# Kernel tuning notes

Measured on AMD Instinct MI355X. Metric: run time of the kernel, lower is better.

Reference implementation:

```python
import jax, jax.numpy as jnp
import numpy as np

V, E, H, L, B, T = 32000, 256, 512, 128, 16, 128


def _gru_scan(x_emb, h0, W_ih, b_ih, W_hh, b_hh):
    # x_emb: [T, B, E] time-major; torch GRU gate order (r, z, n)
    gx = jnp.einsum('tbe,ge->tbg', x_emb, W_ih) + b_ih  # [T, B, 3H]
    def step(h, g):
        gh = h @ W_hh.T + b_hh
        xr, xz, xn = jnp.split(g, 3, axis=-1)
        hr, hz, hn = jnp.split(gh, 3, axis=-1)
        r = jax.nn.sigmoid(xr + hr)
        u = jax.nn.sigmoid(xz + hz)
        n = jnp.tanh(xn + r * hn)
        h_new = (1.0 - u) * n + u * h
        return h_new, h_new
    return jax.lax.scan(step, h0, gx)


def setup_inputs() -> dict:
    key = jax.random.key(0)
    ks = jax.random.split(key, 20)
    s = 0.02
    f = lambda k, shp: jax.random.normal(k, shp, dtype=jnp.float32) * s
    return {
        'x': jax.random.randint(ks[0], (B, T), 0, V),
        'enc_emb': f(ks[1], (V, E)),
        'enc_W_ih': f(ks[2], (3 * H, E)),
        'enc_b_ih': f(ks[3], (3 * H,)),
        'enc_W_hh': f(ks[4], (3 * H, H)),
        'enc_b_hh': f(ks[5], (3 * H,)),
        'fc_enc_W': f(ks[6], (L, H)),
        'fc_enc_b': f(ks[7], (L,)),
        'fc_dec_W': f(ks[8], (H, L)),
        'fc_dec_b': f(ks[9], (H,)),
        'dec_emb': f(ks[10], (V, E)),
        'dec_W_ih': f(ks[11], (3 * H, E)),
        'dec_b_ih': f(ks[12], (3 * H,)),
        'dec_W_hh': f(ks[13], (3 * H, H)),
        'dec_b_hh': f(ks[14], (3 * H,)),
        'dec_fc_W': f(ks[15], (V, H)),
        'dec_fc_b': f(ks[16], (V,)),
    }


def reference(x, enc_emb, enc_W_ih, enc_b_ih, enc_W_hh, enc_b_hh,
              fc_enc_W, fc_enc_b, fc_dec_W, fc_dec_b,
              dec_emb, dec_W_ih, dec_b_ih, dec_W_hh, dec_b_hh,
              dec_fc_W, dec_fc_b):
    Bx, Tx = x.shape
    Hh = enc_W_hh.shape[1]
    # Encoder: GRU over full sequence, take final hidden
    xe = enc_emb[x].transpose(1, 0, 2)                    # [T, B, E]
    h_last, _ = _gru_scan(xe, jnp.zeros((Bx, Hh), xe.dtype),
                          enc_W_ih, enc_b_ih, enc_W_hh, enc_b_hh)
    z = h_last @ fc_enc_W.T + fc_enc_b                    # [B, L]
    hid0 = jnp.tanh(z @ fc_dec_W.T + fc_dec_b)            # [B, H]
    # Decoder with teacher_forcing=1.0: inputs are x[:, 0:T-1]
    de = dec_emb[x[:, :-1]].transpose(1, 0, 2)            # [T-1, B, E]
    _, hs = _gru_scan(de, hid0, dec_W_ih, dec_b_ih, dec_W_hh, dec_b_hh)
    logits = jnp.einsum('tbh,vh->btv', hs, dec_fc_W) + dec_fc_b  # [B, T-1, V]
    Vv = dec_fc_W.shape[0]
    outputs = jnp.zeros((Bx, Tx, Vv), logits.dtype).at[:, 1:].set(logits)
    return outputs, z
```

## Files before the change

kernel.cpp:

```cpp
#include <hip/hip_runtime.h>

#define Vv 32000
#define Ee 256
#define Hh 512
#define Ll 128
#define Bb 16
#define Tt 128
#define G3 1536
#define NSW 256
#define NPAIRB (Bb * Hh)

typedef __attribute__((ext_vector_type(8))) short short8;
typedef __attribute__((ext_vector_type(4))) float f32x4;

__device__ __forceinline__ float sigmoidf_(float x) { return 1.f / (1.f + __expf(-x)); }

__device__ __forceinline__ unsigned short f2bf(float f) {
  unsigned int u = __float_as_uint(f);
  u = (u + 0x7fffu + ((u >> 16) & 1u)) >> 16;
  return (unsigned short)u;
}

__global__ void k_zero_first(float* __restrict__ out) {
  int idx = blockIdx.x * 256 + threadIdx.x;
  if (idx < Bb * Vv) {
    int b = idx / Vv, v = idx % Vv;
    out[(size_t)b * Tt * Vv + v] = 0.f;
  }
}

__global__ void k_cvt_bf16(const float* __restrict__ in, unsigned short* __restrict__ out,
                           int n4) {
  int i = blockIdx.x * 256 + threadIdx.x;
  if (i < n4) {
    float4 v = ((const float4*)in)[i];
    ushort4 o;
    o.x = f2bf(v.x); o.y = f2bf(v.y); o.z = f2bf(v.z); o.w = f2bf(v.w);
    ((ushort4*)out)[i] = o;
  }
}

__global__ void k_transpose(const float* __restrict__ in, float* __restrict__ out,
                            int R, int C) {
  __shared__ float tile[32][33];
  int c = blockIdx.x * 32 + threadIdx.x;
  int r0 = blockIdx.y * 32;
  for (int i = threadIdx.y; i < 32; i += 8)
    tile[i][threadIdx.x] = in[(size_t)(r0 + i) * C + c];
  __syncthreads();
  int r = r0 + threadIdx.x;
  int c0 = blockIdx.x * 32;
  for (int i = threadIdx.y; i < 32; i += 8)
    out[(size_t)(c0 + i) * R + r] = tile[threadIdx.x][i];
}

__device__ __forceinline__ void gx_body(int e, const int* __restrict__ x,
                                        const float* __restrict__ emb,
                                        const float* __restrict__ WihT,
                                        const float* __restrict__ b_ih,
                                        float* __restrict__ gx) {
  __shared__ float A[16][Ee];
  int mt = e / 6, gy = e % 6;
  int g = gy * 256 + threadIdx.x;
  for (int i = 0; i < 16; i++) {
    int tok = x[i * Tt + mt];
    A[i][threadIdx.x] = emb[(size_t)tok * Ee + threadIdx.x];
  }
  __syncthreads();
  float acc[16];
  float bg = b_ih[g];
#pragma unroll
  for (int i = 0; i < 16; i++) acc[i] = bg;
#pragma unroll 4
  for (int ee = 0; ee < Ee; ee++) {
    float w = WihT[(size_t)ee * G3 + g];
#pragma unroll
    for (int i = 0; i < 16; i++) acc[i] = fmaf(A[i][ee], w, acc[i]);
  }
#pragma unroll
  for (int i = 0; i < 16; i++)
    gx[(size_t)(mt * 16 + i) * G3 + g] = acc[i];
}

__global__ void k_gx(const int* __restrict__ x, const float* __restrict__ emb,
                     const float* __restrict__ WihT, const float* __restrict__ b_ih,
                     float* __restrict__ gx) {
  gx_body(blockIdx.x, x, emb, WihT, b_ih, gx);
}

template <bool HSEQ>
__device__ __forceinline__ void scan_body(
    const float* __restrict__ Whh, const float* __restrict__ bhh,
    const float* __restrict__ gx, uint2* __restrict__ pairs,
    unsigned short* __restrict__ hseq, int nsteps) {
  __shared__ float h_lds[Hh];
  const int tid = threadIdx.x;
  const int wg = blockIdx.x;
  const int g = wg >> 4;
  const int wgl = wg & 15;
  const int wave = tid >> 6;
  const int lane = tid & 63;
  const int cl = lane >> 3;
  const int ks = lane & 7;
  const int j = wgl * 32 + wave * 8 + cl;
  const bool gate = (ks == 0);

  float wr[64], wz[64], wn[64];
  {
    const float* R = Whh + (size_t)j * Hh + ks * 4;
    const float* Z = R + (size_t)Hh * Hh;
    const float* N = Z + (size_t)Hh * Hh;
#pragma unroll
    for (int q = 0; q < 16; ++q) {
      float4 a = *(const float4*)(R + q * 32);
      float4 b = *(const float4*)(Z + q * 32);
      float4 c = *(const float4*)(N + q * 32);
      wr[4*q] = a.x; wr[4*q+1] = a.y; wr[4*q+2] = a.z; wr[4*q+3] = a.w;
      wz[4*q] = b.x; wz[4*q+1] = b.y; wz[4*q+2] = b.z; wz[4*q+3] = b.w;
      wn[4*q] = c.x; wn[4*q+1] = c.y; wn[4*q+2] = c.z; wn[4*q+3] = c.w;
    }
  }
  float bhr = 0.f, bhz = 0.f, bhn = 0.f;
  if (gate) { bhr = bhh[j]; bhz = bhh[Hh + j]; bhn = bhh[2 * Hh + j]; }

  float xr = 0.f, xz = 0.f, xn = 0.f;
  if (gate) {
    const float* gp = gx + (size_t)g * G3 + j;
    xr = gp[0]; xz = gp[Hh]; xn = gp[2 * Hh];
  }

  for (int t = 0; t < nsteps; ++t) {
    {
      const uint4* pp =
          (const uint4*)(pairs + (size_t)(t & 1) * NPAIRB + (size_t)g * Hh) + tid;
      const unsigned ep = (unsigned)t;
      uint4 v;
      for (int it = 0; it < 200000; ++it) {
        asm volatile("global_load_dwordx4 %0, %1, off sc1\n\ts_waitcnt vmcnt(0)"
                     : "=v"(v) : "v"(pp) : "memory");
        if (v.y == ep && v.w == ep) break;
      }
      *(float2*)&h_lds[2 * tid] =
          make_float2(__uint_as_float(v.x), __uint_as_float(v.z));
    }
    __syncthreads();

    float aR = 0.f, aZ = 0.f, aN = 0.f;
    {
      const float* hb = h_lds + ks * 4;
#pragma unroll
      for (int q = 0; q < 16; ++q) {
        float4 hv = *(const float4*)(hb + q * 32);
        aR = fmaf(wr[4*q+0], hv.x, aR);
        aR = fmaf(wr[4*q+1], hv.y, aR);
        aR = fmaf(wr[4*q+2], hv.z, aR);
        aR = fmaf(wr[4*q+3], hv.w, aR);
        aZ = fmaf(wz[4*q+0], hv.x, aZ);
        aZ = fmaf(wz[4*q+1], hv.y, aZ);
        aZ = fmaf(wz[4*q+2], hv.z, aZ);
        aZ = fmaf(wz[4*q+3], hv.w, aZ);
        aN = fmaf(wn[4*q+0], hv.x, aN);
        aN = fmaf(wn[4*q+1], hv.y, aN);
        aN = fmaf(wn[4*q+2], hv.z, aN);
        aN = fmaf(wn[4*q+3], hv.w, aN);
      }
    }
    aR += __shfl_xor(aR, 1, 64); aR += __shfl_xor(aR, 2, 64); aR += __shfl_xor(aR, 4, 64);
    aZ += __shfl_xor(aZ, 1, 64); aZ += __shfl_xor(aZ, 2, 64); aZ += __shfl_xor(aZ, 4, 64);
    aN += __shfl_xor(aN, 1, 64); aN += __shfl_xor(aN, 2, 64); aN += __shfl_xor(aN, 4, 64);

    if (gate) {
      float r = sigmoidf_(xr + aR + bhr);
      float u = sigmoidf_(xz + aZ + bhz);
      float n = tanhf(xn + r * (aN + bhn));
      float hold = h_lds[j];
      float hnew = (1.f - u) * n + u * hold;
      uint2 pv = make_uint2(__float_as_uint(hnew), (unsigned)(t + 1));
      uint2* dst = pairs + (size_t)((t + 1) & 1) * NPAIRB + (size_t)g * Hh + j;
      asm volatile("global_store_dwordx2 %0, %1, off sc1" : : "v"(dst), "v"(pv) : "memory");
      if (HSEQ) hseq[((size_t)t * Bb + g) * Hh + j] = f2bf(hnew);
      if (t + 1 < nsteps) {
        const float* gp = gx + (size_t)((t + 1) * Bb + g) * G3 + j;
        xr = gp[0]; xz = gp[Hh]; xn = gp[2 * Hh];
      }
    }
    __syncthreads();
  }
}

__global__ void __launch_bounds__(256, 1) k_enc_fused(
    const float* __restrict__ Whh, const float* __restrict__ bhh,
    const float* __restrict__ gx_e, uint2* __restrict__ pairs,
    const int* __restrict__ x, const float* __restrict__ dec_emb,
    const float* __restrict__ wihT_d, const float* __restrict__ dec_bih,
    float* __restrict__ gx_d) {
  if (blockIdx.x < NSW)
    scan_body<false>(Whh, bhh, gx_e, pairs, (unsigned short*)nullptr, Tt);
  else
    gx_body(blockIdx.x - NSW, x, dec_emb, wihT_d, dec_bih, gx_d);
}

__global__ void __launch_bounds__(256, 1) k_dec_scan(
    const float* __restrict__ Whh, const float* __restrict__ bhh,
    const float* __restrict__ gx_d, uint2* __restrict__ pairs,
    unsigned short* __restrict__ hseq) {
  scan_body<true>(Whh, bhh, gx_d, pairs, hseq, Tt - 1);
}

__global__ void k_zh(const uint2* __restrict__ hp,
                     const float* __restrict__ Wz, const float* __restrict__ bz,
                     float* __restrict__ zout,
                     const float* __restrict__ Wh, const float* __restrict__ bh,
                     uint2* __restrict__ hp0) {
  int b = blockIdx.x;
  int tid = threadIdx.x;
  __shared__ float hsh[Hh];
  __shared__ float zsh[Ll];
  hsh[tid] = __uint_as_float(hp[b * Hh + tid].x);
  __syncthreads();
  if (tid < Ll) {
    float acc = bz[tid];
#pragma unroll 4
    for (int k = 0; k < Hh; k++) acc = fmaf(hsh[k], Wz[(size_t)tid * Hh + k], acc);
    zsh[tid] = acc;
    zout[b * Ll + tid] = acc;
  }
  __syncthreads();
  float acc = bh[tid];
#pragma unroll 4
  for (int l = 0; l < Ll; l++) acc = fmaf(zsh[l], Wh[(size_t)tid * Ll + l], acc);
  hp0[b * Hh + tid] = make_uint2(__float_as_uint(tanhf(acc)), 0u);
}

template <bool BF16W>
__global__ void __launch_bounds__(256) k_logits_mfma(
    const unsigned short* __restrict__ Abf,
    const unsigned short* __restrict__ Wbf,
    const float* __restrict__ Wf,
    const float* __restrict__ bias, float* __restrict__ out) {
  const int tid = threadIdx.x;
  const int wid = tid >> 6, lane = tid & 63;
  const int ln = lane & 15, hi = lane >> 4;
  const int n0 = blockIdx.x * 64;
  const int m0 = blockIdx.y * 256 + wid * 64;
  f32x4 acc[4][4];
#pragma unroll
  for (int mi = 0; mi < 4; ++mi)
#pragma unroll
    for (int ni = 0; ni < 4; ++ni) acc[mi][ni] = (f32x4)0.f;

  const unsigned short* hp = Abf + (size_t)(m0 + ln) * Hh + hi * 8;
  const unsigned short* wp16 = BF16W ? (Wbf + (size_t)(n0 + ln) * Hh + hi * 8) : nullptr;
  const float* wp32 = BF16W ? nullptr : (Wf + (size_t)(n0 + ln) * Hh + hi * 8);

  for (int kt = 0; kt < 16; ++kt) {
    short8 aW[4], bH[4];
#pragma unroll
    for (int ni = 0; ni < 4; ++ni) {
      if (BF16W) {
        aW[ni] = *(const short8*)(wp16 + (size_t)ni * 16 * Hh + kt * 32);
      } else {
        const float* q = wp32 + (size_t)ni * 16 * Hh + kt * 32;
        short8 tv;
#pragma unroll
        for (int e = 0; e < 8; ++e) tv[e] = (short)f2bf(q[e]);
        aW[ni] = tv;
      }
    }
#pragma unroll
    for (int mi = 0; mi < 4; ++mi)
      bH[mi] = *(const short8*)(hp + (size_t)mi * 16 * Hh + kt * 32);
#pragma unroll
    for (int mi = 0; mi < 4; ++mi)
#pragma unroll
      for (int ni = 0; ni < 4; ++ni)
        acc[mi][ni] = __builtin_amdgcn_mfma_f32_16x16x32_bf16(aW[ni], bH[mi], acc[mi][ni], 0, 0, 0);
  }

#pragma unroll
  for (int ni = 0; ni < 4; ++ni) {
    const int n = n0 + ni * 16 + hi * 4;
    const f32x4 bv = *(const f32x4*)&bias[n];
#pragma unroll
    for (int mi = 0; mi < 4; ++mi) {
      int m = m0 + mi * 16 + ln;
      if (m < 2032) {
        int t = m >> 4, bb = m & 15;
        float* dst = out + ((size_t)(bb * Tt + 1 + t)) * Vv + n;
        f32x4 o = acc[mi][ni] + bv;
        __builtin_nontemporal_store(o, (f32x4*)dst);
      }
    }
  }
}

extern "C" void kernel_launch(void* const* d_in, const int* in_sizes, int n_in,
                              void* d_out, int out_size, void* d_ws, size_t ws_size,
                              hipStream_t stream) {
  const int* x = (const int*)d_in[0];
  const float* enc_emb = (const float*)d_in[1];
  const float* enc_Wih = (const float*)d_in[2];
  const float* enc_bih = (const float*)d_in[3];
  const float* enc_Whh = (const float*)d_in[4];
  const float* enc_bhh = (const float*)d_in[5];
  const float* fc_enc_W = (const float*)d_in[6];
  const float* fc_enc_b = (const float*)d_in[7];
  const float* fc_dec_W = (const float*)d_in[8];
  const float* fc_dec_b = (const float*)d_in[9];
  const float* dec_emb = (const float*)d_in[10];
  const float* dec_Wih = (const float*)d_in[11];
  const float* dec_bih = (const float*)d_in[12];
  const float* dec_Whh = (const float*)d_in[13];
  const float* dec_bhh = (const float*)d_in[14];
  const float* dec_fcW = (const float*)d_in[15];
  const float* dec_fcb = (const float*)d_in[16];
  float* out = (float*)d_out;

  float* ws = (float*)d_ws;
  size_t off = 0;
  float* wihT_e = ws + off; off += 393216;
  float* wihT_d = ws + off; off += 393216;
  float* gx_e = ws + off; off += 3145728;
  float* gx_d = ws + off; off += 3121152;
  uint2* enc_pairs = (uint2*)(ws + off); off += 4 * NPAIRB;
  uint2* dec_pairs = (uint2*)(ws + off); off += 4 * NPAIRB;
  unsigned short* hseq_bf = (unsigned short*)(ws + off); off += 524288;
  size_t wbf_elems = (size_t)Vv * Hh;
  bool use_wbf = (off + wbf_elems / 2) * sizeof(float) <= ws_size;
  unsigned short* wbf = (unsigned short*)(ws + off);

  hipMemsetAsync(enc_pairs, 0, 8 * NPAIRB * sizeof(uint2) / 2, stream);
  k_zero_first<<<(Bb * Vv + 255) / 256, 256, 0, stream>>>(out);

  if (use_wbf)
    k_cvt_bf16<<<(int)((wbf_elems / 4 + 255) / 256), 256, 0, stream>>>(
        dec_fcW, wbf, (int)(wbf_elems / 4));

  dim3 tb(32, 8);
  k_transpose<<<dim3(256 / 32, 1536 / 32), tb, 0, stream>>>(enc_Wih, wihT_e, 1536, 256);
  k_transpose<<<dim3(256 / 32, 1536 / 32), tb, 0, stream>>>(dec_Wih, wihT_d, 1536, 256);

  k_gx<<<128 * 6, 256, 0, stream>>>(x, enc_emb, wihT_e, enc_bih, gx_e);

  k_enc_fused<<<NSW + 762, 256, 0, stream>>>(enc_Whh, enc_bhh, gx_e, enc_pairs,
                                             x, dec_emb, wihT_d, dec_bih, gx_d);

  k_zh<<<16, 512, 0, stream>>>(enc_pairs, fc_enc_W, fc_enc_b,
                               out + (size_t)Bb * Tt * Vv, fc_dec_W, fc_dec_b, dec_pairs);

  k_dec_scan<<<NSW, 256, 0, stream>>>(dec_Whh, dec_bhh, gx_d, dec_pairs, hseq_bf);

  if (use_wbf)
    k_logits_mfma<true><<<dim3(Vv / 64, 8), 256, 0, stream>>>(hseq_bf, wbf, dec_fcW,
                                                              dec_fcb, out);
  else
    k_logits_mfma<false><<<dim3(Vv / 64, 8), 256, 0, stream>>>(hseq_bf, (unsigned short*)nullptr,
                                                               dec_fcW, dec_fcb, out);
}
```

Baseline: 830.9 us.

## Stage logits weight tile in LDS and loop all M rows per block

```diff
diff --git a/kernel.cpp b/kernel.cpp
--- a/kernel.cpp
+++ b/kernel.cpp
@@ -233,62 +233,77 @@
 }
 
 template <bool BF16W>
-__global__ void __launch_bounds__(256) k_logits_mfma(
+__global__ void __launch_bounds__(512, 1) k_logits_mfma(
     const unsigned short* __restrict__ Abf,
     const unsigned short* __restrict__ Wbf,
     const float* __restrict__ Wf,
     const float* __restrict__ bias, float* __restrict__ out) {
+  __shared__ short W_lds[32768];
   const int tid = threadIdx.x;
-  const int wid = tid >> 6, lane = tid & 63;
+  const int wave = tid >> 6, lane = tid & 63;
   const int ln = lane & 15, hi = lane >> 4;
   const int n0 = blockIdx.x * 64;
-  const int m0 = blockIdx.y * 256 + wid * 64;
-  f32x4 acc[4][4];
-#pragma unroll
-  for (int mi = 0; mi < 4; ++mi)
-#pragma unroll
-    for (int ni = 0; ni < 4; ++ni) acc[mi][ni] = (f32x4)0.f;
-
-  const unsigned short* hp = Abf + (size_t)(m0 + ln) * Hh + hi * 8;
-  const unsigned short* wp16 = BF16W ? (Wbf + (size_t)(n0 + ln) * Hh + hi * 8) : nullptr;
-  const float* wp32 = BF16W ? nullptr : (Wf + (size_t)(n0 + ln) * Hh + hi * 8);
-
-  for (int kt = 0; kt < 16; ++kt) {
-    short8 aW[4], bH[4];
+
+#pragma unroll
+  for (int c = 0; c < 8; ++c) {
+    int f = c * 512 + tid;
+    int row = f & 63;
+    int kc = f >> 6;
+    short8 v;
+    if (BF16W) {
+      v = *(const short8*)(Wbf + (size_t)(n0 + row) * Hh + kc * 8);
+    } else {
+      const float* q = Wf + (size_t)(n0 + row) * Hh + kc * 8;
+      short8 tv;
+#pragma unroll
+      for (int e = 0; e < 8; ++e) tv[e] = (short)f2bf(q[e]);
+      v = tv;
+    }
+    *(short8*)&W_lds[f * 8] = v;
+  }
+  __syncthreads();
+
+  f32x4 bv[4];
+#pragma unroll
+  for (int ni = 0; ni < 4; ++ni)
+    bv[ni] = *(const f32x4*)&bias[n0 + ni * 16 + hi * 4];
+
+  for (int pass = 0; pass < 4; ++pass) {
+    const int m0 = pass * 512 + wave * 64;
+    const unsigned short* hp = Abf + (size_t)(m0 + ln) * Hh + hi * 8;
+    f32x4 acc[4][4];
+#pragma unroll
+    for (int mi = 0; mi < 4; ++mi)
+#pragma unroll
+      for (int ni = 0; ni < 4; ++ni) acc[mi][ni] = (f32x4)0.f;
+
+    for (int kt = 0; kt < 16; ++kt) {
+      short8 aW[4], bH[4];
+#pragma unroll
+      for (int ni = 0; ni < 4; ++ni)
+        aW[ni] = *(const short8*)&W_lds[(((kt * 4 + hi) * 64) + ni * 16 + ln) * 8];
+#pragma unroll
+      for (int mi = 0; mi < 4; ++mi)
+        bH[mi] = *(const short8*)(hp + (size_t)mi * 16 * Hh + kt * 32);
+#pragma unroll
+      for (int mi = 0; mi < 4; ++mi)
+#pragma unroll
+        for (int ni = 0; ni < 4; ++ni)
+          acc[mi][ni] = __builtin_amdgcn_mfma_f32_16x16x32_bf16(aW[ni], bH[mi], acc[mi][ni], 0, 0, 0);
+    }
+
 #pragma unroll
     for (int ni = 0; ni < 4; ++ni) {
-      if (BF16W) {
-        aW[ni] = *(const short8*)(wp16 + (size_t)ni * 16 * Hh + kt * 32);
-      } else {
-        const float* q = wp32 + (size_t)ni * 16 * Hh + kt * 32;
-        short8 tv;
-#pragma unroll
-        for (int e = 0; e < 8; ++e) tv[e] = (short)f2bf(q[e]);
-        aW[ni] = tv;
-      }
-    }
-#pragma unroll
-    for (int mi = 0; mi < 4; ++mi)
-      bH[mi] = *(const short8*)(hp + (size_t)mi * 16 * Hh + kt * 32);
-#pragma unroll
-    for (int mi = 0; mi < 4; ++mi)
-#pragma unroll
-      for (int ni = 0; ni < 4; ++ni)
-        acc[mi][ni] = __builtin_amdgcn_mfma_f32_16x16x32_bf16(aW[ni], bH[mi], acc[mi][ni], 0, 0, 0);
-  }
-
-#pragma unroll
-  for (int ni = 0; ni < 4; ++ni) {
-    const int n = n0 + ni * 16 + hi * 4;
-    const f32x4 bv = *(const f32x4*)&bias[n];
-#pragma unroll
-    for (int mi = 0; mi < 4; ++mi) {
-      int m = m0 + mi * 16 + ln;
-      if (m < 2032) {
-        int t = m >> 4, bb = m & 15;
-        float* dst = out + ((size_t)(bb * Tt + 1 + t)) * Vv + n;
-        f32x4 o = acc[mi][ni] + bv;
-        __builtin_nontemporal_store(o, (f32x4*)dst);
+      const int n = n0 + ni * 16 + hi * 4;
+#pragma unroll
+      for (int mi = 0; mi < 4; ++mi) {
+        int m = m0 + mi * 16 + ln;
+        if (m < 2032) {
+          int t = m >> 4, bb = m & 15;
+          float* dst = out + ((size_t)(bb * Tt + 1 + t)) * Vv + n;
+          f32x4 o = acc[mi][ni] + bv[ni];
+          __builtin_nontemporal_store(o, (f32x4*)dst);
+        }
       }
     }
   }
@@ -351,9 +366,8 @@
   k_dec_scan<<<NSW, 256, 0, stream>>>(dec_Whh, dec_bhh, gx_d, dec_pairs, hseq_bf);
 
   if (use_wbf)
-    k_logits_mfma<true><<<dim3(Vv / 64, 8), 256, 0, stream>>>(hseq_bf, wbf, dec_fcW,
-                                                              dec_fcb, out);
+    k_logits_mfma<true><<<500, 512, 0, stream>>>(hseq_bf, wbf, dec_fcW, dec_fcb, out);
   else
-    k_logits_mfma<false><<<dim3(Vv / 64, 8), 256, 0, stream>>>(hseq_bf, (unsigned short*)nullptr,
-                                                               dec_fcW, dec_fcb, out);
-}
+    k_logits_mfma<false><<<500, 512, 0, stream>>>(hseq_bf, (unsigned short*)nullptr,
+                                                  dec_fcW, dec_fcb, out);
+}
```

Measured after the change: 703.3 us. -15.4%, faster.
